# Kernel optimization log

Measured on AMD Instinct MI355X. Metric: run time of the kernel, lower is better.

The kernel has to match this reference:

```python
import jax, jax.numpy as jnp
import numpy as np

B, N, M, D, NH, HD = 2, 1024, 1024, 1536, 16, 96
RD = HD // 3  # per-axis rotary dim = 32
EPS = 1e-6
SCALE = HD ** -0.5


def _rmsnorm(y, w):
    return y * jax.lax.rsqrt(jnp.mean(y * y, axis=-1, keepdims=True) + EPS) * w


def _rope_tables(T, H, W):
    # inv_freqs identical for t/h/w since all three dims are RD
    inv_f = 1.0 / (10000.0 ** (jnp.arange(0, RD, 2, dtype=jnp.float32)[: RD // 2] / RD))
    gt, gh, gw = jnp.meshgrid(
        jnp.arange(T, dtype=jnp.float32),
        jnp.arange(H, dtype=jnp.float32),
        jnp.arange(W, dtype=jnp.float32),
        indexing='ij')
    ft = gt.reshape(-1, 1) * inv_f[None, :]  # [L, RD//2]
    fh = gh.reshape(-1, 1) * inv_f[None, :]
    fw = gw.reshape(-1, 1) * inv_f[None, :]
    return (jnp.cos(ft), jnp.sin(ft), jnp.cos(fh), jnp.sin(fh), jnp.cos(fw), jnp.sin(fw))


def _apply_rope(xq, cos, sin):
    # xq: [B, L, NH, RD]; cos/sin: [L, RD//2]
    c = jnp.concatenate([cos, cos], axis=-1)[None, :, None, :]
    s = jnp.concatenate([sin, sin], axis=-1)[None, :, None, :]
    x1, x2 = jnp.split(xq, 2, axis=-1)
    rot = jnp.concatenate([-x2, x1], axis=-1)
    return xq * c + rot * s


def setup_inputs() -> dict:
    key = jax.random.key(0)
    ks = jax.random.split(key, 10)
    w = lambda k: jax.random.normal(k, (D, D), dtype=jnp.float32) * 0.02
    return {
        'cond': jax.random.normal(ks[0], (B, N, D), dtype=jnp.float32),
        'x': jax.random.normal(ks[1], (B, M, D), dtype=jnp.float32),
        'cond_q_w': w(ks[2]), 'cond_k_w': w(ks[3]), 'cond_v_w': w(ks[4]),
        'cond_qnorm_w': jnp.ones((D,), jnp.float32),
        'cond_knorm_w': jnp.ones((D,), jnp.float32),
        'cond_proj_w': w(ks[5]),
        'x_q_w': w(ks[6]), 'x_k_w': w(ks[7]), 'x_v_w': w(ks[8]),
        'x_qnorm_w': jnp.ones((D,), jnp.float32),
        'x_knorm_w': jnp.ones((D,), jnp.float32),
        'x_proj_w': w(ks[9]),
        'T': 2, 'H': 32, 'W': 32,
    }


def reference(cond, x, cond_q_w, cond_k_w, cond_v_w, cond_qnorm_w, cond_knorm_w,
              cond_proj_w, x_q_w, x_k_w, x_v_w, x_qnorm_w, x_knorm_w, x_proj_w,
              T, H, W):
    # dual-stream QKV + RMSNorm (qkv_bias=False, eval -> no dropout)
    cq = _rmsnorm(cond @ cond_q_w, cond_qnorm_w).reshape(B, N, NH, HD)
    ck = _rmsnorm(cond @ cond_k_w, cond_knorm_w).reshape(B, N, NH, HD)
    cv = (cond @ cond_v_w).reshape(B, N, NH, HD)
    xq = _rmsnorm(x @ x_q_w, x_qnorm_w).reshape(B, M, NH, HD)
    xk = _rmsnorm(x @ x_k_w, x_knorm_w).reshape(B, M, NH, HD)
    xv = (x @ x_v_w).reshape(B, M, NH, HD)

    q = jnp.concatenate([cq, xq], axis=1)  # [B, N+M, NH, HD]
    k = jnp.concatenate([ck, xk], axis=1)
    v = jnp.concatenate([cv, xv], axis=1)

    # 3D RoPE: split head_dim into t/h/w thirds and rotate each with its own freqs
    cos_t, sin_t, cos_h, sin_h, cos_w, sin_w = _rope_tables(T, H, W)
    qt, qh, qw = jnp.split(q, 3, axis=-1)
    kt, kh, kw = jnp.split(k, 3, axis=-1)
    q = jnp.concatenate([_apply_rope(qt, cos_t, sin_t),
                         _apply_rope(qh, cos_h, sin_h),
                         _apply_rope(qw, cos_w, sin_w)], axis=-1)
    k = jnp.concatenate([_apply_rope(kt, cos_t, sin_t),
                         _apply_rope(kh, cos_h, sin_h),
                         _apply_rope(kw, cos_w, sin_w)], axis=-1)

    # joint non-causal SDPA
    scores = jnp.einsum('blhd,bmhd->bhlm', q, k) * SCALE
    attn = jax.nn.softmax(scores, axis=-1)
    out = jnp.einsum('bhlm,bmhd->blhd', attn, v).reshape(B, N + M, D)

    cond_out = out[:, :N] @ cond_proj_w
    x_out = out[:, N:] @ x_proj_w
    return cond_out, x_out
```

## Files before the change

### kernel.cpp

```cpp
#include <hip/hip_runtime.h>
#include <stdint.h>

#define DEV __device__ __forceinline__

using f32x4  = __attribute__((ext_vector_type(4))) float;
using f32x16 = __attribute__((ext_vector_type(16))) float;
using bf16x8 = __attribute__((ext_vector_type(8))) short;

DEV ushort f2bf(float f){
  uint32_t u = __float_as_uint(f);
  u += 0x7FFFu + ((u >> 16) & 1u);
  return (ushort)(u >> 16);
}
DEV float bf2f(ushort h){ return __uint_as_float(((uint32_t)h) << 16); }

DEV void async16(const void* g, void* l){
  __builtin_amdgcn_global_load_lds(
      (const __attribute__((address_space(1))) void*)g,
      (__attribute__((address_space(3))) void*)l, 16, 0, 0);
}

union FU { uint4 u; bf16x8 v; };
DEV bf16x8 as_bf16x8(uint a, uint b, uint c, uint d){ FU f; f.u = make_uint4(a,b,c,d); return f.v; }

__global__ __launch_bounds__(256) void k_conv_in(const float* __restrict__ src, ushort* __restrict__ dst){
  int i = (blockIdx.x * 256 + threadIdx.x) * 8;
  float4 a = *(const float4*)(src + i);
  float4 b = *(const float4*)(src + i + 4);
  union { ushort s[8]; uint4 q; } o;
  o.s[0]=f2bf(a.x); o.s[1]=f2bf(a.y); o.s[2]=f2bf(a.z); o.s[3]=f2bf(a.w);
  o.s[4]=f2bf(b.x); o.s[5]=f2bf(b.y); o.s[6]=f2bf(b.z); o.s[7]=f2bf(b.w);
  *(uint4*)(dst + i) = o.q;
}

__global__ __launch_bounds__(256) void k_transpose_w(
    const float* w0, const float* w1, const float* w2, const float* w3,
    const float* w4, const float* w5, const float* w6, const float* w7,
    ushort* __restrict__ dst){
  __shared__ float tile[32][33];
  int z = blockIdx.z;
  const float* src = (z==0)?w0:(z==1)?w1:(z==2)?w2:(z==3)?w3:(z==4)?w4:(z==5)?w5:(z==6)?w6:w7;
  int n0 = blockIdx.x * 32;
  int k0 = blockIdx.y * 32;
  int tx = threadIdx.x;
  int ty = threadIdx.y;
  for (int j = 0; j < 4; ++j)
    tile[ty + j*8][tx] = src[(size_t)(k0 + ty + j*8) * 1536 + n0 + tx];
  __syncthreads();
  ushort* d = dst + (size_t)z * 1536 * 1536;
  for (int j = 0; j < 4; ++j){
    int n = n0 + ty + j*8;
    int k = k0 + tx;
    d[(size_t)n * 1536 + k] = f2bf(tile[tx][ty + j*8]);
  }
}

__global__ __launch_bounds__(512, 2) void k_gemm_qkv(const ushort* __restrict__ inb,
                                                     const ushort* __restrict__ Wt,
                                                     ushort* __restrict__ Y){
  __shared__ ushort As[2][16384];
  __shared__ ushort Bs[2][18432];
  int f = blockIdx.x;
  int nid = (f & 7) * 32 + (f >> 3);
  int z = nid >> 7; int r = nid & 127;
  int my = (r >> 2) & 7, nx = (r >> 5) * 4 + (r & 3);
  const ushort* A = inb + (size_t)z * 2048 * 1536 + (size_t)(my * 256) * 1536;
  const ushort* B = Wt  + (size_t)z * 4608 * 1536 + (size_t)(nx * 288) * 1536;
  ushort* Yt = Y + (size_t)z * 2048 * 4608 + (size_t)(my * 256) * 4608 + nx * 288;
  int tid = threadIdx.x;
  int w = tid >> 6, lane = tid & 63;
  int g = lane >> 4, fr = lane & 15;
  int wm = (w >> 1) * 64, wn = (w & 1) * 144;

  f32x4 acc[4][9] = {};

  auto stageA = [&](int b, int kt){
#pragma unroll
    for (int s = 0; s < 4; ++s){
      int c = s * 512 + tid;
      int row = c >> 3, ch = c & 7;
      async16(A + (size_t)row * 1536 + kt + ((ch ^ (row & 7)) * 8), &As[b][(s*512 + w*64) * 8]);
    }
  };
  auto stageB = [&](int b, int kt){
#pragma unroll
    for (int s = 0; s < 4; ++s){
      int c = s * 512 + tid;
      int row = c >> 3, ch = c & 7;
      async16(B + (size_t)row * 1536 + kt + ((ch ^ (row & 7)) * 8), &Bs[b][(s*512 + w*64) * 8]);
    }
    if (tid < 256){
      int c = 2048 + tid;
      int row = c >> 3, ch = c & 7;
      async16(B + (size_t)row * 1536 + kt + ((ch ^ (row & 7)) * 8), &Bs[b][(2048 + w*64) * 8]);
    }
  };

  stageA(0, 0); stageB(0, 0);
  asm volatile("s_waitcnt vmcnt(0)" ::: "memory");
  __builtin_amdgcn_s_barrier();
  asm volatile("" ::: "memory");

  for (int t = 0; t < 24; ++t){
    int cur = t & 1; int kt1 = (t + 1) * 64;
#pragma unroll
    for (int ks = 0; ks < 2; ++ks){
      bf16x8 af[4], bf[9];
#pragma unroll
      for (int j = 0; j < 4; ++j){
        int row = wm + j*16 + fr;
        af[j] = *(const bf16x8*)&As[cur][(row*8 + ((ks*4 + g) ^ (row & 7))) * 8];
      }
#pragma unroll
      for (int ni = 0; ni < 9; ++ni){
        int row = wn + ni*16 + fr;
        bf[ni] = *(const bf16x8*)&Bs[cur][(row*8 + ((ks*4 + g) ^ (row & 7))) * 8];
      }
      if (t < 23){
        if (ks == 0) stageA(cur ^ 1, kt1);
        else stageB(cur ^ 1, kt1);
      }
      asm volatile("" ::: "memory");
      __builtin_amdgcn_s_barrier();
      asm volatile("" ::: "memory");
      __builtin_amdgcn_s_setprio(1);
#pragma unroll
      for (int ni = 0; ni < 9; ++ni){
#pragma unroll
        for (int j = 0; j < 4; ++j)
          acc[j][ni] = __builtin_amdgcn_mfma_f32_16x16x32_bf16(af[j], bf[ni], acc[j][ni], 0, 0, 0);
      }
      __builtin_amdgcn_s_setprio(0);
      if (ks == 1) asm volatile("s_waitcnt vmcnt(0)" ::: "memory");
      asm volatile("" ::: "memory");
      __builtin_amdgcn_s_barrier();
      asm volatile("" ::: "memory");
    }
  }

#pragma unroll
  for (int mi = 0; mi < 4; ++mi)
#pragma unroll
    for (int ni = 0; ni < 9; ++ni)
#pragma unroll
      for (int rr = 0; rr < 4; ++rr)
        Yt[(size_t)(wm + mi*16 + g*4 + rr) * 4608 + wn + ni*16 + fr] = f2bf(acc[mi][ni][rr]);
}

template<bool OUT_BF16>
DEV void gemm_tile(const ushort* __restrict__ A, const ushort* __restrict__ Bt, void* __restrict__ Cp,
                   int K, int lda, int ldb, int ldc, int m0, int n0){
  __shared__ ushort As[8192];
  __shared__ ushort Bs[8192];
  int tid = threadIdx.x;
  int w = tid >> 6, lane = tid & 63;
  int g = lane >> 4, fr = lane & 15;
  int wm = (w >> 1) * 64, wn = (w & 1) * 64;
  f32x4 acc[4][4] = {};
  for (int kt = 0; kt < K; kt += 64){
    __syncthreads();
#pragma unroll
    for (int i = 0; i < 4; ++i){
      int ci = i * 256 + tid;
      int row = ci >> 3, ch = ci & 7;
      int src8 = (ch ^ (row & 7)) * 8;
      async16(A  + (size_t)(m0 + row) * lda + kt + src8, As + (i*256 + w*64) * 8);
      async16(Bt + (size_t)(n0 + row) * ldb + kt + src8, Bs + (i*256 + w*64) * 8);
    }
    __syncthreads();
#pragma unroll
    for (int ks = 0; ks < 2; ++ks){
      bf16x8 af[4], bf[4];
      int cidx = ((ks*4 + g) ^ (fr & 7)) * 8;
#pragma unroll
      for (int mi = 0; mi < 4; ++mi) af[mi] = *(const bf16x8*)(As + (wm + mi*16 + fr) * 64 + cidx);
#pragma unroll
      for (int ni = 0; ni < 4; ++ni) bf[ni] = *(const bf16x8*)(Bs + (wn + ni*16 + fr) * 64 + cidx);
#pragma unroll
      for (int mi = 0; mi < 4; ++mi)
#pragma unroll
        for (int ni = 0; ni < 4; ++ni)
          acc[mi][ni] = __builtin_amdgcn_mfma_f32_16x16x32_bf16(af[mi], bf[ni], acc[mi][ni], 0, 0, 0);
    }
  }
  int cr = (lane >> 4) * 4, cc2 = lane & 15;
#pragma unroll
  for (int mi = 0; mi < 4; ++mi)
#pragma unroll
    for (int ni = 0; ni < 4; ++ni)
#pragma unroll
      for (int r = 0; r < 4; ++r){
        size_t idx = (size_t)(m0 + wm + mi*16 + cr + r) * ldc + (n0 + wn + ni*16 + cc2);
        if (OUT_BF16) ((ushort*)Cp)[idx] = f2bf(acc[mi][ni][r]);
        else          ((float*)Cp)[idx]  = acc[mi][ni][r];
      }
}

__global__ __launch_bounds__(256) void k_gemm_proj(const ushort* __restrict__ AO, const ushort* __restrict__ Wtp,
                                                   float* __restrict__ out){
  int f = blockIdx.x;
  int nid = (f & 7) * 48 + (f >> 3);
  int z = nid / 96; int rr = nid - z * 96;
  int by = rr / 12; int bx = rr - by * 12;
  int s = z >> 1, bb = z & 1;
  gemm_tile<false>(AO + (size_t)(bb*2048 + s*1024) * 1536, Wtp + (size_t)s * 1536 * 1536,
                   (void*)(out + (size_t)(s*2048 + bb*1024) * 1536), 1536, 1536, 1536, 1536,
                   by * 128, bx * 128);
}

__global__ __launch_bounds__(256) void k_norm_rope(
    const ushort* __restrict__ Y,
    const float* __restrict__ qn_c, const float* __restrict__ kn_c,
    const float* __restrict__ qn_x, const float* __restrict__ kn_x,
    ushort* __restrict__ Qb, ushort* __restrict__ Kb){
  int r = blockIdx.x;
  int z = blockIdx.y;
  const ushort* y = Y + ((size_t)z * 2048 + r) * 4608;
  const float* qw = z ? qn_x : qn_c;
  const float* kw = z ? kn_x : kn_c;
  int b = r >> 10;
  int l = (z << 10) + (r & 1023);
  int tid = threadIdx.x;
  __shared__ float cs[48], sn[48];
  if (tid < 48){
    int axis = tid >> 4, fj = tid & 15;
    int pos = (axis == 0) ? (l >> 10) : ((axis == 1) ? ((l >> 5) & 31) : (l & 31));
    float inv = __expf(-(float)fj * 0.5756462732485114f);
    float a = (float)pos * inv;
    sn[tid] = sinf(a); cs[tid] = cosf(a);
  }
  float yq1[3], yq2[3], yk1[3], yk2[3];
  float ssq = 0.f, ssk = 0.f;
#pragma unroll
  for (int i = 0; i < 3; ++i){
    int p = tid + i*256;
    int head = p / 48, rem = p % 48;
    int c1 = head*96 + (rem >> 4)*32 + (rem & 15);
    float a1 = bf2f(y[c1]),        a2 = bf2f(y[c1 + 16]);
    float b1 = bf2f(y[1536 + c1]), b2 = bf2f(y[1536 + c1 + 16]);
    yq1[i]=a1; yq2[i]=a2; yk1[i]=b1; yk2[i]=b2;
    ssq += a1*a1 + a2*a2;
    ssk += b1*b1 + b2*b2;
  }
#pragma unroll
  for (int mm = 1; mm < 64; mm <<= 1){
    ssq += __shfl_xor(ssq, mm);
    ssk += __shfl_xor(ssk, mm);
  }
  __shared__ float red[8];
  int w = tid >> 6;
  if ((tid & 63) == 0){ red[w] = ssq; red[4 + w] = ssk; }
  __syncthreads();
  float scq = rsqrtf((red[0]+red[1]+red[2]+red[3]) * (1.f/1536.f) + 1e-6f);
  float sck = rsqrtf((red[4]+red[5]+red[6]+red[7]) * (1.f/1536.f) + 1e-6f);
  float scqS = scq * 0.1020620726159658f;
#pragma unroll
  for (int i = 0; i < 3; ++i){
    int p = tid + i*256;
    int head = p / 48, rem = p % 48;
    int axis = rem >> 4, fj = rem & 15;
    int c1 = head*96 + axis*32 + fj;
    float c = cs[rem], s = sn[rem];
    size_t rowb = ((size_t)(b*16 + head) * 2048 + l) * 96;
    float a1 = yq1[i] * scqS * qw[c1], a2 = yq2[i] * scqS * qw[c1 + 16];
    Qb[rowb + axis*32 + fj]      = f2bf(a1*c - a2*s);
    Qb[rowb + axis*32 + fj + 16] = f2bf(a2*c + a1*s);
    float b1 = yk1[i] * sck * kw[c1], b2 = yk2[i] * sck * kw[c1 + 16];
    int d1 = axis*32 + fj;
    Kb[rowb + d1]      = f2bf(b1*c - b2*s);
    Kb[rowb + d1 + 16] = f2bf(b2*c + b1*s);
  }
}

__global__ __launch_bounds__(256) void k_transpose_v(const ushort* __restrict__ Y, ushort* __restrict__ Vt){
  __shared__ ushort t[32][33];
  int bh = blockIdx.z;
  int b = bh >> 4, head = bh & 15;
  int c0 = blockIdx.x * 32;
  int l0 = blockIdx.y * 32;
  int z = l0 >> 10;
  const ushort* src = Y + ((size_t)(z*2048 + b*1024 + (l0 & 1023))) * 4608 + 3072 + head*96 + c0;
  ushort* dst = Vt + (size_t)bh * 96 * 2048;
  int tx = threadIdx.x, ty = threadIdx.y;
  for (int j = 0; j < 4; ++j)
    t[ty + j*8][tx] = src[(size_t)(ty + j*8) * 4608 + tx];
  __syncthreads();
  for (int j = 0; j < 4; ++j)
    dst[(size_t)(c0 + ty + j*8) * 2048 + l0 + tx] = t[tx][ty + j*8];
}

__global__ __launch_bounds__(256, 2) void k_attn(const ushort* __restrict__ Qb, const ushort* __restrict__ Kb,
                                                 const ushort* __restrict__ Vt, ushort* __restrict__ AO){
  __shared__ ushort Ks[2][6400];
  __shared__ ushort Vs[2][6528];
  int id = blockIdx.x;
  int nid = (id & 7) * 64 + (id >> 3);
  int qt = nid & 15, bh = nid >> 4;
  int b = bh >> 4, head = bh & 15;
  const ushort* Qh = Qb + (size_t)bh * 2048 * 96;
  const ushort* Kh = Kb + (size_t)bh * 2048 * 96;
  const ushort* Vh = Vt + (size_t)bh * 96 * 2048;
  int tid = threadIdx.x;
  int w = tid >> 6, lane = tid & 63;
  int h = lane >> 5, c = lane & 31;
  int q0 = qt * 128 + w * 32;

  bf16x8 qf[6];
#pragma unroll
  for (int kb = 0; kb < 6; ++kb)
    qf[kb] = *(const bf16x8*)(Qh + (size_t)(q0 + c) * 96 + kb*16 + h*8);

  int gko[3], lko[3], gvo[3], lvo[3];
#pragma unroll
  for (int i = 0; i < 3; ++i){
    int fc = i*256 + tid;
    int krow = (fc * 683) >> 13;
    int kc8  = (fc - krow*12) * 8;
    gko[i] = krow*96 + kc8;
    lko[i] = krow*100 + kc8;
    int vrow = fc >> 3;
    int vc8  = (fc & 7) * 8;
    gvo[i] = vrow*2048 + vc8;
    lvo[i] = vrow*68 + (vc8 ^ ((vrow & 7) << 3));
  }
  uint4 kst[3], vst[3];
  f32x16 o[3] = {};
  float dpart = 0.f;
  f32x16 sa[2];

  auto LOADG = [&](int tt){
#pragma unroll
    for (int i = 0; i < 3; ++i){
      kst[i] = *(const uint4*)(Kh + (size_t)tt*6144 + gko[i]);
      vst[i] = *(const uint4*)(Vh + (size_t)tt*64 + gvo[i]);
    }
  };
  auto WRITE = [&](int buf){
#pragma unroll
    for (int i = 0; i < 3; ++i){
      *(uint2*)(&Ks[buf][lko[i]])     = make_uint2(kst[i].x, kst[i].y);
      *(uint2*)(&Ks[buf][lko[i] + 4]) = make_uint2(kst[i].z, kst[i].w);
      *(uint2*)(&Vs[buf][lvo[i]])     = make_uint2(vst[i].x, vst[i].y);
      *(uint2*)(&Vs[buf][lvo[i] + 4]) = make_uint2(vst[i].z, vst[i].w);
    }
  };
  auto QK = [&](f32x16* out, int buf){
#pragma unroll
    for (int ni = 0; ni < 2; ++ni){
      f32x16 a = {};
#pragma unroll
      for (int kb = 0; kb < 6; ++kb){
        const ushort* kp = &Ks[buf][(ni*32 + c)*100 + kb*16 + h*8];
        uint2 lo = *(const uint2*)kp;
        uint2 hi = *(const uint2*)(kp + 4);
        a = __builtin_amdgcn_mfma_f32_32x32x16_bf16(as_bf16x8(lo.x, lo.y, hi.x, hi.y), qf[kb], a, 0, 0, 0);
      }
      out[ni] = a;
    }
  };

  LOADG(0);
  WRITE(0);
  LOADG(1);
  asm volatile("s_waitcnt lgkmcnt(0)" ::: "memory");
  __builtin_amdgcn_s_barrier();
  asm volatile("" ::: "memory");
  QK(sa, 0);

  for (int t = 0; t < 32; ++t){
    int cur = t & 1, nxt = cur ^ 1;
    if (t < 31) WRITE(nxt);
    if (t < 30) LOADG(t + 2);
    asm volatile("s_waitcnt lgkmcnt(0)" ::: "memory");
    __builtin_amdgcn_s_barrier();
    asm volatile("" ::: "memory");

    bf16x8 pf[2][2];
#pragma unroll
    for (int ni = 0; ni < 2; ++ni){
      float p[16];
#pragma unroll
      for (int e = 0; e < 16; ++e){
        float x = fmaf(sa[ni][e], 1.44269504f, -14.4269504f);
        asm("v_exp_f32 %0, %1" : "=v"(p[e]) : "v"(x));
      }
      dpart += (((p[0]+p[1])+(p[2]+p[3])) + ((p[4]+p[5])+(p[6]+p[7])))
             + (((p[8]+p[9])+(p[10]+p[11])) + ((p[12]+p[13])+(p[14]+p[15])));
      uint u[8];
#pragma unroll
      for (int e = 0; e < 8; ++e)
        asm("v_cvt_pk_bf16_f32 %0, %1, %2" : "=v"(u[e]) : "v"(p[2*e]), "v"(p[2*e+1]));
      asm("v_permlane32_swap_b32 %0, %1" : "+v"(u[0]), "+v"(u[2]));
      asm("v_permlane32_swap_b32 %0, %1" : "+v"(u[1]), "+v"(u[3]));
      asm("v_permlane32_swap_b32 %0, %1" : "+v"(u[4]), "+v"(u[6]));
      asm("v_permlane32_swap_b32 %0, %1" : "+v"(u[5]), "+v"(u[7]));
      pf[ni][0] = as_bf16x8(u[0], u[1], u[2], u[3]);
      pf[ni][1] = as_bf16x8(u[4], u[5], u[6], u[7]);
    }

    __builtin_amdgcn_s_setprio(1);
    if (t < 31){
      f32x16 na[2];
      QK(na, nxt);
#pragma unroll
      for (int dt = 0; dt < 3; ++dt)
#pragma unroll
        for (int ni = 0; ni < 2; ++ni)
#pragma unroll
          for (int ks = 0; ks < 2; ++ks){
            int chunk = 4*ni + 2*ks + h;
            const ushort* vp = &Vs[cur][(dt*32 + c)*68 + ((chunk ^ (c & 7)) << 3)];
            uint2 lo = *(const uint2*)vp;
            uint2 hi = *(const uint2*)(vp + 4);
            o[dt] = __builtin_amdgcn_mfma_f32_32x32x16_bf16(pf[ni][ks],
                      as_bf16x8(lo.x, lo.y, hi.x, hi.y), o[dt], 0, 0, 0);
          }
      sa[0] = na[0]; sa[1] = na[1];
    } else {
#pragma unroll
      for (int dt = 0; dt < 3; ++dt)
#pragma unroll
        for (int ni = 0; ni < 2; ++ni)
#pragma unroll
          for (int ks = 0; ks < 2; ++ks){
            int chunk = 4*ni + 2*ks + h;
            const ushort* vp = &Vs[cur][(dt*32 + c)*68 + ((chunk ^ (c & 7)) << 3)];
            uint2 lo = *(const uint2*)vp;
            uint2 hi = *(const uint2*)(vp + 4);
            o[dt] = __builtin_amdgcn_mfma_f32_32x32x16_bf16(pf[ni][ks],
                      as_bf16x8(lo.x, lo.y, hi.x, hi.y), o[dt], 0, 0, 0);
          }
    }
    __builtin_amdgcn_s_setprio(0);
    asm volatile("" ::: "memory");
    __builtin_amdgcn_s_barrier();
    asm volatile("" ::: "memory");
  }

  float dtot = dpart + __shfl_xor(dpart, 32);
#pragma unroll
  for (int r = 0; r < 16; ++r){
    int qloc = (r & 3) + 8*(r >> 2) + 4*h;
    float den = __shfl(dtot, qloc);
    float dinv = __builtin_amdgcn_rcpf(den);
    size_t rowoff = ((size_t)b * 2048 + q0 + qloc) * 1536 + head * 96;
#pragma unroll
    for (int dt = 0; dt < 3; ++dt){
      float val = o[dt][r] * dinv;
      uint pk; asm("v_cvt_pk_bf16_f32 %0, %1, %2" : "=v"(pk) : "v"(val), "v"(val));
      AO[rowoff + dt*32 + c] = (ushort)pk;
    }
  }
}

extern "C" void kernel_launch(void* const* d_in, const int* in_sizes, int n_in,
                              void* d_out, int out_size, void* d_ws, size_t ws_size,
                              hipStream_t stream){
  const float* cond = (const float*)d_in[0];
  const float* x    = (const float*)d_in[1];
  const float* wq_c = (const float*)d_in[2];
  const float* wk_c = (const float*)d_in[3];
  const float* wv_c = (const float*)d_in[4];
  const float* qn_c = (const float*)d_in[5];
  const float* kn_c = (const float*)d_in[6];
  const float* wp_c = (const float*)d_in[7];
  const float* wq_x = (const float*)d_in[8];
  const float* wk_x = (const float*)d_in[9];
  const float* wv_x = (const float*)d_in[10];
  const float* qn_x = (const float*)d_in[11];
  const float* kn_x = (const float*)d_in[12];
  const float* wp_x = (const float*)d_in[13];

  char* ws = (char*)d_ws;
  ushort* inb = (ushort*)(ws);
  ushort* Wt  = (ushort*)(ws + 12582912ll);
  ushort* Y   = (ushort*)(ws + 50331648ll);
  ushort* Qb  = (ushort*)(ws + 88080384ll);
  ushort* Kb  = (ushort*)(ws + 100663296ll);
  ushort* Vt  = (ushort*)(ws + 113246208ll);
  ushort* AO  = inb;

  k_conv_in<<<1536, 256, 0, stream>>>(cond, inb);
  k_conv_in<<<1536, 256, 0, stream>>>(x, inb + 3145728);
  k_transpose_w<<<dim3(48,48,8), dim3(32,8), 0, stream>>>(wq_c, wk_c, wv_c, wq_x, wk_x, wv_x, wp_c, wp_x, Wt);
  k_gemm_qkv<<<256, 512, 0, stream>>>(inb, Wt, Y);
  k_norm_rope<<<dim3(2048,2), 256, 0, stream>>>(Y, qn_c, kn_c, qn_x, kn_x, Qb, Kb);
  k_transpose_v<<<dim3(3,64,32), dim3(32,8), 0, stream>>>(Y, Vt);
  k_attn<<<512, 256, 0, stream>>>(Qb, Kb, Vt, AO);
  k_gemm_proj<<<384, 256, 0, stream>>>(AO, Wt + (size_t)9216*1536, (float*)d_out);
  (void)in_sizes; (void)n_in; (void)out_size; (void)ws_size;
}
```

Baseline: 206.9 us.

## Triple-buffer QKV GEMM with 32-wide K tiles and split B fragment loads

Reworks the QKV projection GEMM pipeline from double-buffered 64-wide K steps to triple-buffered 32-wide K steps, prefetching two tiles ahead with a vmcnt(5) wait so global loads overlap more compute. B fragments are loaded in two halves with staged async copies between them, which lowers register pressure per phase. Launch bounds drop to one block per CU because LDS use changes. Separately, the s_setprio raise around the attention kernel's MFMA section is removed. The risk is more barriers per K step and lower occupancy.

Result: no change. 206.1 us (-0.4%).

```diff
diff --git a/kernel.cpp b/kernel.cpp
--- a/kernel.cpp
+++ b/kernel.cpp
@@ -55,11 +55,11 @@
   }
 }
 
-__global__ __launch_bounds__(512, 2) void k_gemm_qkv(const ushort* __restrict__ inb,
+__global__ __launch_bounds__(512, 1) void k_gemm_qkv(const ushort* __restrict__ inb,
                                                      const ushort* __restrict__ Wt,
                                                      ushort* __restrict__ Y){
-  __shared__ ushort As[2][16384];
-  __shared__ ushort Bs[2][18432];
+  __shared__ ushort As[3][8192];
+  __shared__ ushort Bs[3][9216];
   int f = blockIdx.x;
   int nid = (f & 7) * 32 + (f >> 3);
   int z = nid >> 7; int r = nid & 127;
@@ -74,68 +74,73 @@
 
   f32x4 acc[4][9] = {};
 
-  auto stageA = [&](int b, int kt){
-#pragma unroll
-    for (int s = 0; s < 4; ++s){
-      int c = s * 512 + tid;
-      int row = c >> 3, ch = c & 7;
-      async16(A + (size_t)row * 1536 + kt + ((ch ^ (row & 7)) * 8), &As[b][(s*512 + w*64) * 8]);
-    }
+  auto stageA = [&](int buf, int kt, int round){
+    int c = round * 512 + tid;
+    int row = c >> 2, ch = c & 3;
+    async16(A + (size_t)row * 1536 + kt + ((ch ^ (row & 3)) * 8), &As[buf][c * 8]);
   };
-  auto stageB = [&](int b, int kt){
-#pragma unroll
-    for (int s = 0; s < 4; ++s){
-      int c = s * 512 + tid;
-      int row = c >> 3, ch = c & 7;
-      async16(B + (size_t)row * 1536 + kt + ((ch ^ (row & 7)) * 8), &Bs[b][(s*512 + w*64) * 8]);
-    }
-    if (tid < 256){
-      int c = 2048 + tid;
-      int row = c >> 3, ch = c & 7;
-      async16(B + (size_t)row * 1536 + kt + ((ch ^ (row & 7)) * 8), &Bs[b][(2048 + w*64) * 8]);
-    }
+  auto stageB = [&](int buf, int kt, int round){
+    int c = (round == 2) ? (1024 + (tid & 127)) : (round * 512 + tid);
+    int row = c >> 2, ch = c & 3;
+    async16(B + (size_t)row * 1536 + kt + ((ch ^ (row & 3)) * 8), &Bs[buf][c * 8]);
   };
 
-  stageA(0, 0); stageB(0, 0);
-  asm volatile("s_waitcnt vmcnt(0)" ::: "memory");
+  stageA(0, 0, 0); stageA(0, 0, 1); stageB(0, 0, 0); stageB(0, 0, 1); stageB(0, 0, 2);
+  stageA(1, 32, 0); stageA(1, 32, 1); stageB(1, 32, 0); stageB(1, 32, 1); stageB(1, 32, 2);
+  asm volatile("s_waitcnt vmcnt(5)" ::: "memory");
   __builtin_amdgcn_s_barrier();
   asm volatile("" ::: "memory");
 
-  for (int t = 0; t < 24; ++t){
-    int cur = t & 1; int kt1 = (t + 1) * 64;
-#pragma unroll
-    for (int ks = 0; ks < 2; ++ks){
-      bf16x8 af[4], bf[9];
-#pragma unroll
-      for (int j = 0; j < 4; ++j){
-        int row = wm + j*16 + fr;
-        af[j] = *(const bf16x8*)&As[cur][(row*8 + ((ks*4 + g) ^ (row & 7))) * 8];
-      }
-#pragma unroll
-      for (int ni = 0; ni < 9; ++ni){
-        int row = wn + ni*16 + fr;
-        bf[ni] = *(const bf16x8*)&Bs[cur][(row*8 + ((ks*4 + g) ^ (row & 7))) * 8];
-      }
-      if (t < 23){
-        if (ks == 0) stageA(cur ^ 1, kt1);
-        else stageB(cur ^ 1, kt1);
-      }
-      asm volatile("" ::: "memory");
-      __builtin_amdgcn_s_barrier();
-      asm volatile("" ::: "memory");
-      __builtin_amdgcn_s_setprio(1);
-#pragma unroll
-      for (int ni = 0; ni < 9; ++ni){
-#pragma unroll
-        for (int j = 0; j < 4; ++j)
-          acc[j][ni] = __builtin_amdgcn_mfma_f32_16x16x32_bf16(af[j], bf[ni], acc[j][ni], 0, 0, 0);
-      }
-      __builtin_amdgcn_s_setprio(0);
-      if (ks == 1) asm volatile("s_waitcnt vmcnt(0)" ::: "memory");
-      asm volatile("" ::: "memory");
-      __builtin_amdgcn_s_barrier();
-      asm volatile("" ::: "memory");
-    }
+  for (int t = 0; t < 48; ++t){
+    int cb = t % 3, nb2 = (t + 2) % 3;
+    int kt2 = (t + 2) * 32;
+    bf16x8 af[4], bfx[5];
+#pragma unroll
+    for (int j = 0; j < 4; ++j){
+      int row = wm + j*16 + fr;
+      af[j] = *(const bf16x8*)&As[cb][row*32 + ((g ^ (row & 3)) << 3)];
+    }
+#pragma unroll
+    for (int n = 0; n < 5; ++n){
+      int row = wn + n*16 + fr;
+      bfx[n] = *(const bf16x8*)&Bs[cb][row*32 + ((g ^ (row & 3)) << 3)];
+    }
+    if (t < 46){ stageA(nb2, kt2, 0); stageA(nb2, kt2, 1); stageB(nb2, kt2, 0); }
+    asm volatile("" ::: "memory");
+    __builtin_amdgcn_s_barrier();
+    asm volatile("s_waitcnt lgkmcnt(0)" ::: "memory");
+    __builtin_amdgcn_s_setprio(1);
+#pragma unroll
+    for (int n = 0; n < 5; ++n)
+#pragma unroll
+      for (int j = 0; j < 4; ++j)
+        acc[j][n] = __builtin_amdgcn_mfma_f32_16x16x32_bf16(af[j], bfx[n], acc[j][n], 0, 0, 0);
+    __builtin_amdgcn_s_setprio(0);
+    asm volatile("" ::: "memory");
+    __builtin_amdgcn_s_barrier();
+    asm volatile("" ::: "memory");
+    bf16x8 bfy[4];
+#pragma unroll
+    for (int n = 0; n < 4; ++n){
+      int row = wn + (5 + n)*16 + fr;
+      bfy[n] = *(const bf16x8*)&Bs[cb][row*32 + ((g ^ (row & 3)) << 3)];
+    }
+    if (t < 46){ stageB(nb2, kt2, 1); stageB(nb2, kt2, 2); }
+    asm volatile("" ::: "memory");
+    __builtin_amdgcn_s_barrier();
+    asm volatile("s_waitcnt lgkmcnt(0)" ::: "memory");
+    __builtin_amdgcn_s_setprio(1);
+#pragma unroll
+    for (int n = 0; n < 4; ++n)
+#pragma unroll
+      for (int j = 0; j < 4; ++j)
+        acc[j][5 + n] = __builtin_amdgcn_mfma_f32_16x16x32_bf16(af[j], bfy[n], acc[j][5 + n], 0, 0, 0);
+    __builtin_amdgcn_s_setprio(0);
+    if (t < 46)      asm volatile("s_waitcnt vmcnt(5)" ::: "memory");
+    else if (t == 46) asm volatile("s_waitcnt vmcnt(0)" ::: "memory");
+    asm volatile("" ::: "memory");
+    __builtin_amdgcn_s_barrier();
+    asm volatile("" ::: "memory");
   }
 
 #pragma unroll
@@ -398,7 +403,6 @@
       pf[ni][1] = as_bf16x8(u[4], u[5], u[6], u[7]);
     }
 
-    __builtin_amdgcn_s_setprio(1);
     if (t < 31){
       f32x16 na[2];
       QK(na, nxt);
@@ -431,7 +435,6 @@
                       as_bf16x8(lo.x, lo.y, hi.x, hi.y), o[dt], 0, 0, 0);
           }
     }
-    __builtin_amdgcn_s_setprio(0);
     asm volatile("" ::: "memory");
     __builtin_amdgcn_s_barrier();
     asm volatile("" ::: "memory");
```
